# Kernel optimization log

Hardware: AMD Instinct MI355X
Metric: run time of the kernel (lower is better)

Reference implementation:

```python
import jax, jax.numpy as jnp
import numpy as np

D_MODEL = 1024
NHEAD = 16
HEAD_DIM = D_MODEL // NHEAD
LN_EPS = 1e-5


def setup_inputs() -> dict:
    key = jax.random.key(0)
    ks = jax.random.split(key, 6)
    B, S = 4, 4096
    x = jax.random.normal(ks[0], (B, S, D_MODEL), dtype=jnp.float32)
    scale = 0.02
    Wq = jax.random.normal(ks[1], (D_MODEL, D_MODEL), dtype=jnp.float32) * scale
    Wv = jax.random.normal(ks[2], (D_MODEL, D_MODEL), dtype=jnp.float32) * scale
    Wo = jax.random.normal(ks[3], (D_MODEL, D_MODEL), dtype=jnp.float32) * scale
    Wg = jax.random.normal(ks[4], (D_MODEL, D_MODEL), dtype=jnp.float32) * scale
    beta = jnp.full((NHEAD,), -0.2, dtype=jnp.float32)
    ln_gamma = jnp.ones((D_MODEL,), dtype=jnp.float32)
    ln_beta = jnp.zeros((D_MODEL,), dtype=jnp.float32)
    return {"x": x, "Wq": Wq, "Wv": Wv, "Wo": Wo, "Wg": Wg,
            "beta": beta, "ln_gamma": ln_gamma, "ln_beta": ln_beta}


def _ema_scan(lam, v):
    # v: [B, S, H, D]; lam: [1, 1, H, 1]
    # s_t = lam * s_{t-1} + v_t, computed with a parallel associative scan
    # on pairs (a, b) representing the affine map s -> a*s + b.
    a = jnp.broadcast_to(lam, v.shape)

    def combine(e1, e2):
        a1, b1 = e1
        a2, b2 = e2
        return a1 * a2, a2 * b1 + b2

    _, state = jax.lax.associative_scan(combine, (a, v), axis=1)
    return state


def reference(x, Wq, Wv, Wo, Wg, beta, ln_gamma, ln_beta):
    B, S, _ = x.shape
    q = (x @ Wq.T).reshape(B, S, NHEAD, HEAD_DIM)
    v = (x @ Wv.T).reshape(B, S, NHEAD, HEAD_DIM)
    lam = jax.nn.sigmoid(beta).reshape(1, 1, NHEAD, 1).astype(v.dtype)
    state = _ema_scan(lam, v)                      # [B, S, H, D]
    y = (q * state).reshape(B, S, D_MODEL)
    # LayerNorm over last dim
    mu = jnp.mean(y, axis=-1, keepdims=True)
    var = jnp.mean(jnp.square(y - mu), axis=-1, keepdims=True)
    y = (y - mu) * jax.lax.rsqrt(var + LN_EPS) * ln_gamma + ln_beta
    gate = jax.nn.silu(x @ Wg.T)
    y = y * gate
    return y @ Wo.T
```

## Files before the change

### kernel.cpp

```cpp
#include <hip/hip_runtime.h>

#define D_MODEL 1024
#define NHEAD 16
#define LN_EPS 1e-5f
#define CHUNK 32
#define S_LEN 4096
#define NCH (S_LEN / CHUNK)

typedef unsigned short u16;
typedef __attribute__((ext_vector_type(8))) short short8;
typedef __attribute__((ext_vector_type(4))) float f32x4;

__device__ __forceinline__ u16 f2b(float f) {
  unsigned u = __builtin_bit_cast(unsigned, f);
  u += 0x7FFFu + ((u >> 16) & 1u);
  return (u16)(u >> 16);
}
__device__ __forceinline__ float b2f(u16 s) {
  return __builtin_bit_cast(float, ((unsigned)s) << 16);
}

__device__ __forceinline__ ushort4 cvt4(float4 f) {
  ushort4 o; o.x = f2b(f.x); o.y = f2b(f.y); o.z = f2b(f.z); o.w = f2b(f.w);
  return o;
}
__global__ __launch_bounds__(256) void cvt_all(
    const float4* __restrict__ x,  const float4* __restrict__ wq,
    const float4* __restrict__ wv, const float4* __restrict__ wg,
    const float4* __restrict__ wo, ushort4* __restrict__ xb,
    ushort4* __restrict__ wqvg, ushort4* __restrict__ wob,
    const float* __restrict__ beta, float* __restrict__ lam,
    int nx4, int nw4) {
  int i = blockIdx.x * blockDim.x + threadIdx.x;
  int stride = gridDim.x * blockDim.x;
  if (blockIdx.x == 0 && threadIdx.x < NHEAD) {
    float l = 1.f / (1.f + __expf(-beta[threadIdx.x]));
    lam[threadIdx.x] = l;
    lam[NHEAD + threadIdx.x] = __log2f(l);
  }
  for (int j = i; j < nx4; j += stride) xb[j] = cvt4(x[j]);
  for (int j = i; j < nw4; j += stride) wqvg[j] = cvt4(wq[j]);
  for (int j = i; j < nw4; j += stride) wqvg[nw4 + j] = cvt4(wv[j]);
  for (int j = i; j < nw4; j += stride) wqvg[2 * nw4 + j] = cvt4(wg[j]);
  for (int j = i; j < nw4; j += stride) wob[j] = cvt4(wo[j]);
}


__device__ __forceinline__ void glds16(const u16* g, const u16* l) {
  __builtin_amdgcn_global_load_lds(
      (const __attribute__((address_space(1))) unsigned*)g,
      (__attribute__((address_space(3))) unsigned*)l, 16, 0, 0);
}

#define BAR() asm volatile("s_barrier" ::: "memory")
#define SB0() __builtin_amdgcn_sched_barrier(0)

template <typename OutT, bool CARRY>
__global__ __launch_bounds__(512, 2) void gemm256(const u16* __restrict__ X,
                                                  const u16* __restrict__ W,
                                                  OutT* __restrict__ Out,
                                                  float* __restrict__ carry,
                                                  const float* __restrict__ lamlog,
                                                  int M, int N, int K) {
  __shared__ u16 sm[8][8192];
  const int tid = threadIdx.x;
  const int lane = tid & 63;
  const int wave = tid >> 6;
  const int ln15 = lane & 15, lh = lane >> 4;
  const int wr = wave >> 2, wc = wave & 3;
  const int bm = blockIdx.x * 256, bn = blockIdx.y * 256;
  const int NT = K >> 6;

  const int srow = tid >> 3;
  const int scol = ((tid & 7) ^ (srow & 7)) << 3;
  const u16* Asrc = X + (size_t)(bm + srow) * K + scol;
  const u16* Bsrc = W + (size_t)(bn + srow) * K + scol;
  const int ldsw = wave * 512;

#define STAGE(u, h, tile, src)                                          \
  { const u16* _g = (src) + (size_t)((h) * 128) * K + (tile) * 64;      \
    glds16(_g,                  &sm[u][ldsw]);                          \
    glds16(_g + (size_t)64 * K, &sm[u][ldsw + 4096]); }

  const char* smb = (const char*)&sm[0][0];
  const char* Ard = smb + wr * 16384 + ln15 * 128;
  const char* Brd = smb + (2 + (wc >> 1)) * 16384 + ((wc & 1) * 64 + ln15) * 128;
  const int swz0 = ((lh ^ (ln15 & 7)) << 4);
  const int swz1 = (((4 + lh) ^ (ln15 & 7)) << 4);

#define RD_A(DB, MM, S) (*(const short8*)(Ard + (DB) + (MM) * 2048 + (S)))
#define RD_B(DB, NN, S) (*(const short8*)(Brd + (DB) + (NN) * 2048 + (S)))

  f32x4 acc[8][4];
  f32x4 zero = {0.f, 0.f, 0.f, 0.f};
  #pragma unroll
  for (int m = 0; m < 8; ++m)
    #pragma unroll
    for (int n = 0; n < 4; ++n) acc[m][n] = zero;

  short8 a[8][2], b[4][2];

#define MFMA_Q(M0, N0)                                                        \
  SB0();                                                                      \
  __builtin_amdgcn_s_setprio(1);                                              \
  _Pragma("unroll")                                                           \
  for (int m = (M0); m < (M0) + 4; ++m)                                       \
    _Pragma("unroll")                                                         \
    for (int n = (N0); n < (N0) + 2; ++n) {                                   \
      acc[m][n] = __builtin_amdgcn_mfma_f32_16x16x32_bf16(a[m][0], b[n][0], acc[m][n], 0, 0, 0); \
      acc[m][n] = __builtin_amdgcn_mfma_f32_16x16x32_bf16(a[m][1], b[n][1], acc[m][n], 0, 0, 0); \
    }                                                                         \
  __builtin_amdgcn_s_setprio(0);                                              \
  SB0();

  STAGE(0, 0, 0, Asrc); STAGE(1, 1, 0, Asrc);
  STAGE(2, 0, 0, Bsrc); STAGE(3, 1, 0, Bsrc);
  STAGE(4, 0, 1, Asrc); STAGE(5, 1, 1, Asrc);
  asm volatile("s_waitcnt vmcnt(4)" ::: "memory");
  BAR();
  #pragma unroll
  for (int m = 0; m < 4; ++m) { a[m][0] = RD_A(0, m, swz0); a[m][1] = RD_A(0, m, swz1); }
  #pragma unroll
  for (int n = 0; n < 4; ++n) { b[n][0] = RD_B(0, n, swz0); b[n][1] = RD_B(0, n, swz1); }

  for (int t = 0; t < NT; ++t) {
    const int d = t & 1;
    const int db = d * 65536;
    const int odb = (d ^ 1) * 65536;
    const int od = (d ^ 1) * 4;
    const int sd = d * 4;
    const int tB = (t + 1 < NT) ? t + 1 : NT - 1;
    const int tA = (t + 2 < NT) ? t + 2 : NT - 1;

    a[4][0] = RD_A(db, 4, swz0); a[4][1] = RD_A(db, 4, swz1);
    a[5][0] = RD_A(db, 5, swz0); a[5][1] = RD_A(db, 5, swz1);
    STAGE(od + 2, 0, tB, Bsrc);
    MFMA_Q(0, 0)

    a[6][0] = RD_A(db, 6, swz0); a[6][1] = RD_A(db, 6, swz1);
    a[7][0] = RD_A(db, 7, swz0); a[7][1] = RD_A(db, 7, swz1);
    STAGE(od + 3, 1, tB, Bsrc);
    MFMA_Q(0, 2)
    asm volatile("s_waitcnt vmcnt(4)" ::: "memory");
    BAR();

    #pragma unroll
    for (int m = 0; m < 4; ++m) { a[m][0] = RD_A(odb, m, swz0); a[m][1] = RD_A(odb, m, swz1); }
    MFMA_Q(4, 2)
    STAGE(sd + 0, 0, tA, Asrc);
    asm volatile("s_waitcnt vmcnt(2)" ::: "memory");
    BAR();

    b[2][0] = RD_B(odb, 2, swz0); b[2][1] = RD_B(odb, 2, swz1);
    b[3][0] = RD_B(odb, 3, swz0); b[3][1] = RD_B(odb, 3, swz1);
    MFMA_Q(4, 0)
    b[0][0] = RD_B(odb, 0, swz0); b[0][1] = RD_B(odb, 0, swz1);
    b[1][0] = RD_B(odb, 1, swz0); b[1][1] = RD_B(odb, 1, swz1);
    STAGE(sd + 1, 1, tA, Asrc);
  }
#undef STAGE
#undef RD_A
#undef RD_B
#undef MFMA_Q

  if constexpr (CARRY) {
    if (bn >= 1024 && bn < 2048) {
      const float l2h = lamlog[((bn - 1024) + wc * 64) >> 6];
      const float lp1 = exp2f(l2h);
      const float lp2 = lp1 * lp1, lp3 = lp2 * lp1, lp4 = lp2 * lp2;
      const float l8 = lp4 * lp4;
      const float lpl = exp2f(l2h * (float)(4 * lh));
      #pragma unroll
      for (int q = 0; q < 4; ++q)
        #pragma unroll
        for (int n = 0; n < 4; ++n) {
          f32x4 A0 = acc[2 * q][n], A1 = acc[2 * q + 1][n];
          A0[1] += lp1 * A0[0]; A0[2] += lp1 * A0[1]; A0[3] += lp1 * A0[2];
          A1[1] += lp1 * A1[0]; A1[2] += lp1 * A1[1]; A1[3] += lp1 * A1[2];
          float S = A0[3], x;
          x = __shfl_up(S, 16); if (lh >= 1) S += lp4 * x;
          x = __shfl_up(S, 32); if (lh >= 2) S += l8 * x;
          float Xc = __shfl_up(S, 16); Xc = (lh >= 1) ? Xc : 0.f;
          A0[0] += lp1 * Xc; A0[1] += lp2 * Xc; A0[2] += lp3 * Xc; A0[3] += lp4 * Xc;
          float f15 = __shfl(A0[3], 48 + ln15);
          S = A1[3];
          x = __shfl_up(S, 16); if (lh >= 1) S += lp4 * x;
          x = __shfl_up(S, 32); if (lh >= 2) S += l8 * x;
          Xc = __shfl_up(S, 16); Xc = (lh >= 1) ? Xc : 0.f;
          Xc += lpl * f15;
          A1[0] += lp1 * Xc; A1[1] += lp2 * Xc; A1[2] += lp3 * Xc; A1[3] += lp4 * Xc;
          acc[2 * q][n] = A0; acc[2 * q + 1][n] = A1;
        }
    }
  }

  #pragma unroll
  for (int m = 0; m < 8; ++m)
    #pragma unroll
    for (int n = 0; n < 4; ++n)
      #pragma unroll
      for (int r = 0; r < 4; ++r) {
        int row = bm + wr * 128 + m * 16 + lh * 4 + r;
        int col = bn + wc * 64 + n * 16 + ln15;
        float vv = acc[m][n][r];
        if constexpr (sizeof(OutT) == 2) Out[(size_t)row * N + col] = f2b(vv);
        else                             Out[(size_t)row * N + col] = vv;
      }

  if constexpr (CARRY) {
    if (bn >= 1024 && bn < 2048 && lh == 3) {
      const int bidx = bm >> 12;
      const int chunkbase = ((bm & 4095) >> 5) + wr * 4;
      const int colbase = (bn - 1024) + wc * 64;
      #pragma unroll
      for (int q = 0; q < 4; ++q)
        #pragma unroll
        for (int n = 0; n < 4; ++n)
          carry[(size_t)(bidx * NCH + chunkbase + q) * D_MODEL +
                colbase + n * 16 + ln15] = acc[2 * q + 1][n][3];
    }
  }
}

__global__ void scan_carry(float* __restrict__ carry, const float* __restrict__ lam,
                           int B, int nch) {
  int idx = blockIdx.x * blockDim.x + threadIdx.x;
  if (idx >= B * D_MODEL) return;
  int b = idx >> 10, col = idx & (D_MODEL - 1);
  float lC = exp2f(lam[NHEAD + (col >> 6)] * (float)CHUNK);
  float c = 0.f;
  #pragma unroll 4
  for (int j = 0; j < nch; ++j) {
    size_t a = ((size_t)(b * nch + j)) * D_MODEL + col;
    c = lC * c + carry[a];
    carry[a] = c;
  }
}

__global__ __launch_bounds__(256) void ew_ln(const u16* __restrict__ qvg,
    const float* __restrict__ carry, const float* __restrict__ lam,
    const float* __restrict__ gamma, const float* __restrict__ lbeta,
    u16* __restrict__ yout, int nch, int ld) {
  int row = blockIdx.x;
  int b = row >> 12;
  int srow = row & 4095;
  int j = srow >> 5, tl = srow & 31;
  int tid = threadIdx.x;
  int col0 = tid * 4;
  size_t rb = (size_t)row * ld;

  ushort4 qu = *(const ushort4*)(qvg + rb + col0);
  ushort4 su = *(const ushort4*)(qvg + rb + D_MODEL + col0);
  float st[4] = {b2f(su.x), b2f(su.y), b2f(su.z), b2f(su.w)};
  if (j > 0) {
    float p = exp2f(lam[NHEAD + (col0 >> 6)] * (float)(tl + 1));
    const float4 c4 = *(const float4*)(carry + ((size_t)(b * nch + j - 1)) * D_MODEL + col0);
    st[0] += p * c4.x; st[1] += p * c4.y; st[2] += p * c4.z; st[3] += p * c4.w;
  }
  float q[4] = {b2f(qu.x), b2f(qu.y), b2f(qu.z), b2f(qu.w)};
  float y[4];
  float sum = 0.f, sumsq = 0.f;
  #pragma unroll
  for (int i = 0; i < 4; ++i) {
    y[i] = q[i] * st[i];
    sum += y[i];
    sumsq += y[i] * y[i];
  }
  #pragma unroll
  for (int off = 32; off > 0; off >>= 1) {
    sum += __shfl_down(sum, off);
    sumsq += __shfl_down(sumsq, off);
  }
  __shared__ float red[8];
  int ln = tid & 63, wv = tid >> 6;
  if (ln == 0) { red[wv] = sum; red[4 + wv] = sumsq; }
  __syncthreads();
  sum = red[0] + red[1] + red[2] + red[3];
  sumsq = red[4] + red[5] + red[6] + red[7];
  float mu = sum * (1.f / 1024.f);
  float var = sumsq * (1.f / 1024.f) - mu * mu;
  float rstd = rsqrtf(var + LN_EPS);

  float4 gm = *(const float4*)(gamma + col0);
  float4 bt = *(const float4*)(lbeta + col0);
  ushort4 gu = *(const ushort4*)(qvg + rb + 2 * D_MODEL + col0);
  float gv[4]  = {b2f(gu.x), b2f(gu.y), b2f(gu.z), b2f(gu.w)};
  float gmv[4] = {gm.x, gm.y, gm.z, gm.w};
  float btv[4] = {bt.x, bt.y, bt.z, bt.w};
  u16 ov[4];
  #pragma unroll
  for (int i = 0; i < 4; ++i) {
    float gate = gv[i] / (1.f + __expf(-gv[i]));
    float oo = ((y[i] - mu) * rstd * gmv[i] + btv[i]) * gate;
    ov[i] = f2b(oo);
  }
  ushort4 o; o.x = ov[0]; o.y = ov[1]; o.z = ov[2]; o.w = ov[3];
  *(ushort4*)(yout + (size_t)row * D_MODEL + col0) = o;
}

extern "C" void kernel_launch(void* const* d_in, const int* in_sizes, int n_in,
                              void* d_out, int out_size, void* d_ws, size_t ws_size,
                              hipStream_t stream) {
  const float* x     = (const float*)d_in[0];
  const float* Wq    = (const float*)d_in[1];
  const float* Wv    = (const float*)d_in[2];
  const float* Wo    = (const float*)d_in[3];
  const float* Wg    = (const float*)d_in[4];
  const float* beta  = (const float*)d_in[5];
  const float* gamma = (const float*)d_in[6];
  const float* lbeta = (const float*)d_in[7];
  float* out = (float*)d_out;

  const int BS = in_sizes[0] / D_MODEL;
  const int B = BS / S_LEN;
  const int nch = NCH;
  const size_t nx = (size_t)BS * D_MODEL;
  const size_t nw = (size_t)D_MODEL * D_MODEL;
  const int N3 = 3 * D_MODEL;

  char* w = (char*)d_ws;
  u16* xb   = (u16*)w;  w += nx * 2;
  u16* wqvg = (u16*)w;  w += 3 * nw * 2;
  u16* wob  = (u16*)w;  w += nw * 2;
  u16* qvg  = (u16*)w;  w += (size_t)BS * N3 * 2;
  u16* yb   = (u16*)w;  w += nx * 2;
  float* carry = (float*)w;  w += (size_t)B * nch * D_MODEL * 4;
  float* lam = (float*)w;

  cvt_all<<<2048, 256, 0, stream>>>((const float4*)x, (const float4*)Wq,
      (const float4*)Wv, (const float4*)Wg, (const float4*)Wo,
      (ushort4*)xb, (ushort4*)wqvg, (ushort4*)wob, beta, lam,
      (int)(nx / 4), (int)(nw / 4));

  dim3 g1(BS / 256, N3 / 256);
  gemm256<u16, true><<<g1, 512, 0, stream>>>(xb, wqvg, qvg, carry, lam + NHEAD,
                                             BS, N3, D_MODEL);

  scan_carry<<<(B * D_MODEL + 255) / 256, 256, 0, stream>>>(carry, lam, B, nch);
  ew_ln<<<BS, 256, 0, stream>>>(qvg, carry, lam, gamma, lbeta, yb, nch, N3);

  dim3 g2(BS / 256, D_MODEL / 256);
  gemm256<float, false><<<g2, 512, 0, stream>>>(yb, wob, out, nullptr, nullptr,
                                                BS, D_MODEL, D_MODEL);
}
```

Before: 223.4 us.

## Shrink GEMM tile to 256x128 with 4 waves and BK=32 pipeline

Restructures the bf16 GEMM from a 256x256 tile with 8 waves and a K-step of 64 to a 256x128 tile with 4 waves and a K-step of 32. It uses a new LDS layout and swizzle, and double-buffers A and B with loads issued one tile ahead. This cuts LDS use and doubles the grid size, which should improve occupancy and load balance. In exchange, each tile reuses less data and the loop takes more barriers per unit of work. The CARRY epilogue still assumes the old wave-to-column mapping (wc*64 within bn), which may not match the new 128-wide tile.

Result: slower. 246.1 us (+10.2%).

```diff
diff --git a/kernel.cpp b/kernel.cpp
--- a/kernel.cpp
+++ b/kernel.cpp
@@ -56,40 +56,41 @@
 #define SB0() __builtin_amdgcn_sched_barrier(0)
 
 template <typename OutT, bool CARRY>
-__global__ __launch_bounds__(512, 2) void gemm256(const u16* __restrict__ X,
+__global__ __launch_bounds__(256, 2) void gemm256(const u16* __restrict__ X,
                                                   const u16* __restrict__ W,
                                                   OutT* __restrict__ Out,
                                                   float* __restrict__ carry,
                                                   const float* __restrict__ lamlog,
                                                   int M, int N, int K) {
-  __shared__ u16 sm[8][8192];
+  __shared__ u16 sm[24576];
   const int tid = threadIdx.x;
   const int lane = tid & 63;
   const int wave = tid >> 6;
   const int ln15 = lane & 15, lh = lane >> 4;
-  const int wr = wave >> 2, wc = wave & 3;
-  const int bm = blockIdx.x * 256, bn = blockIdx.y * 256;
-  const int NT = K >> 6;
-
-  const int srow = tid >> 3;
-  const int scol = ((tid & 7) ^ (srow & 7)) << 3;
-  const u16* Asrc = X + (size_t)(bm + srow) * K + scol;
-  const u16* Bsrc = W + (size_t)(bn + srow) * K + scol;
-  const int ldsw = wave * 512;
-
-#define STAGE(u, h, tile, src)                                          \
-  { const u16* _g = (src) + (size_t)((h) * 128) * K + (tile) * 64;      \
-    glds16(_g,                  &sm[u][ldsw]);                          \
-    glds16(_g + (size_t)64 * K, &sm[u][ldsw + 4096]); }
-
-  const char* smb = (const char*)&sm[0][0];
-  const char* Ard = smb + wr * 16384 + ln15 * 128;
-  const char* Brd = smb + (2 + (wc >> 1)) * 16384 + ((wc & 1) * 64 + ln15) * 128;
-  const int swz0 = ((lh ^ (ln15 & 7)) << 4);
-  const int swz1 = (((4 + lh) ^ (ln15 & 7)) << 4);
-
-#define RD_A(DB, MM, S) (*(const short8*)(Ard + (DB) + (MM) * 2048 + (S)))
-#define RD_B(DB, NN, S) (*(const short8*)(Brd + (DB) + (NN) * 2048 + (S)))
+  const int wr = wave >> 1, wc = wave & 1;
+  const int bm = blockIdx.x * 256, bn = blockIdx.y * 128;
+  const int NT = K >> 5;
+
+  const int srow = lane >> 2;
+  const int scol = (((lane & 3) ^ (srow & 3) ^ ((srow >> 2) & 3)) << 3);
+  const u16* Asrc = X + (size_t)(bm + wave * 64 + srow) * K + scol;
+  const u16* Bsrc = W + (size_t)(bn + wave * 32 + srow) * K + scol;
+
+#define STAGE_A(d, tile)                                                      \
+  { const u16* _g = Asrc + (tile) * 32; u16* _l = sm + (d) * 8192 + wave * 2048; \
+    glds16(_g,               _l);        glds16(_g + 16 * K, _l + 512);       \
+    glds16(_g + 32 * K, _l + 1024);      glds16(_g + 48 * K, _l + 1536); }
+#define STAGE_B(d, tile)                                                      \
+  { const u16* _g = Bsrc + (tile) * 32; u16* _l = sm + 16384 + (d) * 4096 + wave * 1024; \
+    glds16(_g, _l); glds16(_g + 16 * K, _l + 512); }
+
+  const char* smb = (const char*)sm;
+  const int cswz = ((lh ^ ((ln15 ^ (ln15 >> 2)) & 3)) << 4);
+  const int Aoff = (wr * 128 + ln15) * 64 + cswz;
+  const int Boff = (wc * 64 + ln15) * 64 + cswz;
+
+#define RD_A(D, MM) (*(const short8*)(smb + (D) * 16384 + Aoff + (MM) * 1024))
+#define RD_B(D, NN) (*(const short8*)(smb + 32768 + (D) * 8192 + Boff + (NN) * 1024))
 
   f32x4 acc[8][4];
   f32x4 zero = {0.f, 0.f, 0.f, 0.f};
@@ -98,70 +99,64 @@
     #pragma unroll
     for (int n = 0; n < 4; ++n) acc[m][n] = zero;
 
-  short8 a[8][2], b[4][2];
-
-#define MFMA_Q(M0, N0)                                                        \
+  short8 a[8], bE[4], bO[4];
+
+#define MFMA_ROWS(M0, BV)                                                     \
   SB0();                                                                      \
   __builtin_amdgcn_s_setprio(1);                                              \
   _Pragma("unroll")                                                           \
   for (int m = (M0); m < (M0) + 4; ++m)                                       \
     _Pragma("unroll")                                                         \
-    for (int n = (N0); n < (N0) + 2; ++n) {                                   \
-      acc[m][n] = __builtin_amdgcn_mfma_f32_16x16x32_bf16(a[m][0], b[n][0], acc[m][n], 0, 0, 0); \
-      acc[m][n] = __builtin_amdgcn_mfma_f32_16x16x32_bf16(a[m][1], b[n][1], acc[m][n], 0, 0, 0); \
-    }                                                                         \
+    for (int n = 0; n < 4; ++n)                                               \
+      acc[m][n] = __builtin_amdgcn_mfma_f32_16x16x32_bf16(a[m], BV[n], acc[m][n], 0, 0, 0); \
   __builtin_amdgcn_s_setprio(0);                                              \
   SB0();
 
-  STAGE(0, 0, 0, Asrc); STAGE(1, 1, 0, Asrc);
-  STAGE(2, 0, 0, Bsrc); STAGE(3, 1, 0, Bsrc);
-  STAGE(4, 0, 1, Asrc); STAGE(5, 1, 1, Asrc);
-  asm volatile("s_waitcnt vmcnt(4)" ::: "memory");
+  STAGE_A(0, 0) STAGE_B(0, 0)
+  STAGE_A(1, 1) STAGE_B(1, 1)
+  asm volatile("s_waitcnt vmcnt(6)" ::: "memory");
   BAR();
   #pragma unroll
-  for (int m = 0; m < 4; ++m) { a[m][0] = RD_A(0, m, swz0); a[m][1] = RD_A(0, m, swz1); }
-  #pragma unroll
-  for (int n = 0; n < 4; ++n) { b[n][0] = RD_B(0, n, swz0); b[n][1] = RD_B(0, n, swz1); }
-
-  for (int t = 0; t < NT; ++t) {
-    const int d = t & 1;
-    const int db = d * 65536;
-    const int odb = (d ^ 1) * 65536;
-    const int od = (d ^ 1) * 4;
-    const int sd = d * 4;
-    const int tB = (t + 1 < NT) ? t + 1 : NT - 1;
-    const int tA = (t + 2 < NT) ? t + 2 : NT - 1;
-
-    a[4][0] = RD_A(db, 4, swz0); a[4][1] = RD_A(db, 4, swz1);
-    a[5][0] = RD_A(db, 5, swz0); a[5][1] = RD_A(db, 5, swz1);
-    STAGE(od + 2, 0, tB, Bsrc);
-    MFMA_Q(0, 0)
-
-    a[6][0] = RD_A(db, 6, swz0); a[6][1] = RD_A(db, 6, swz1);
-    a[7][0] = RD_A(db, 7, swz0); a[7][1] = RD_A(db, 7, swz1);
-    STAGE(od + 3, 1, tB, Bsrc);
-    MFMA_Q(0, 2)
-    asm volatile("s_waitcnt vmcnt(4)" ::: "memory");
+  for (int m = 0; m < 4; ++m) a[m] = RD_A(0, m);
+  #pragma unroll
+  for (int n = 0; n < 4; ++n) bE[n] = RD_B(0, n);
+
+  for (int i = 0; i < NT / 2; ++i) {
+    const int T = 2 * i;
+    const int t2 = (T + 2 < NT) ? T + 2 : NT - 1;
+    const int t3 = (T + 3 < NT) ? T + 3 : NT - 1;
+
+    #pragma unroll
+    for (int m = 4; m < 8; ++m) a[m] = RD_A(0, m);
+    MFMA_ROWS(0, bE)
     BAR();
-
-    #pragma unroll
-    for (int m = 0; m < 4; ++m) { a[m][0] = RD_A(odb, m, swz0); a[m][1] = RD_A(odb, m, swz1); }
-    MFMA_Q(4, 2)
-    STAGE(sd + 0, 0, tA, Asrc);
-    asm volatile("s_waitcnt vmcnt(2)" ::: "memory");
+    STAGE_A(0, t2) STAGE_B(0, t2)
+    asm volatile("s_waitcnt vmcnt(6)" ::: "memory");
     BAR();
-
-    b[2][0] = RD_B(odb, 2, swz0); b[2][1] = RD_B(odb, 2, swz1);
-    b[3][0] = RD_B(odb, 3, swz0); b[3][1] = RD_B(odb, 3, swz1);
-    MFMA_Q(4, 0)
-    b[0][0] = RD_B(odb, 0, swz0); b[0][1] = RD_B(odb, 0, swz1);
-    b[1][0] = RD_B(odb, 1, swz0); b[1][1] = RD_B(odb, 1, swz1);
-    STAGE(sd + 1, 1, tA, Asrc);
-  }
-#undef STAGE
+    #pragma unroll
+    for (int m = 0; m < 4; ++m) a[m] = RD_A(1, m);
+    #pragma unroll
+    for (int n = 0; n < 4; ++n) bO[n] = RD_B(1, n);
+    MFMA_ROWS(4, bE)
+
+    #pragma unroll
+    for (int m = 4; m < 8; ++m) a[m] = RD_A(1, m);
+    MFMA_ROWS(0, bO)
+    BAR();
+    STAGE_A(1, t3) STAGE_B(1, t3)
+    asm volatile("s_waitcnt vmcnt(6)" ::: "memory");
+    BAR();
+    #pragma unroll
+    for (int m = 0; m < 4; ++m) a[m] = RD_A(0, m);
+    #pragma unroll
+    for (int n = 0; n < 4; ++n) bE[n] = RD_B(0, n);
+    MFMA_ROWS(4, bO)
+  }
+#undef STAGE_A
+#undef STAGE_B
 #undef RD_A
 #undef RD_B
-#undef MFMA_Q
+#undef MFMA_ROWS
 
   if constexpr (CARRY) {
     if (bn >= 1024 && bn < 2048) {
@@ -332,14 +327,14 @@
       (ushort4*)xb, (ushort4*)wqvg, (ushort4*)wob, beta, lam,
       (int)(nx / 4), (int)(nw / 4));
 
-  dim3 g1(BS / 256, N3 / 256);
-  gemm256<u16, true><<<g1, 512, 0, stream>>>(xb, wqvg, qvg, carry, lam + NHEAD,
+  dim3 g1(BS / 256, N3 / 128);
+  gemm256<u16, true><<<g1, 256, 0, stream>>>(xb, wqvg, qvg, carry, lam + NHEAD,
                                              BS, N3, D_MODEL);
 
   scan_carry<<<(B * D_MODEL + 255) / 256, 256, 0, stream>>>(carry, lam, B, nch);
   ew_ln<<<BS, 256, 0, stream>>>(qvg, carry, lam, gamma, lbeta, yb, nch, N3);
 
-  dim3 g2(BS / 256, D_MODEL / 256);
-  gemm256<float, false><<<g2, 512, 0, stream>>>(yb, wob, out, nullptr, nullptr,
+  dim3 g2(BS / 256, D_MODEL / 128);
+  gemm256<float, false><<<g2, 256, 0, stream>>>(yb, wob, out, nullptr, nullptr,
                                                 BS, D_MODEL, D_MODEL);
 }
```
